# Optimization experiments

Measured on AMD Instinct MI355X. Metric: run time of the kernel, lower is better.

The kernel has to match this reference:

```python
import jax, jax.numpy as jnp
import numpy as np

B, S, H = 2, 1024, 2048
NH, NKV, HD = 16, 4, 128
KB = 1024
THETA = 10000.0
NREP = NH // NKV
NEG = -1e9


def rotate_half(x):
    x1, x2 = x[..., : HD // 2], x[..., HD // 2 :]
    return jnp.concatenate((-x2, x1), axis=-1)


def setup_inputs() -> dict:
    key = jax.random.key(0)
    ks = jax.random.split(key, 9)
    wscale = 1.0 / np.sqrt(H)
    hidden_states = jax.random.normal(ks[0], (B, S, H), dtype=jnp.float32)
    # causal additive mask over the self-attention block only
    causal = jnp.tril(jnp.ones((S, S), dtype=bool))
    attention_mask = jnp.where(causal, 0.0, NEG).astype(jnp.float32)
    attention_mask = jnp.broadcast_to(attention_mask[None, None], (B, 1, S, S))
    position_ids = jnp.broadcast_to(jnp.arange(S, dtype=jnp.int32)[None], (B, S))
    kb_keys = jax.random.normal(ks[1], (B, KB, NKV * HD), dtype=jnp.float32)
    kb_values = jax.random.normal(ks[2], (B, KB, NKV * HD), dtype=jnp.float32)
    Wq = jax.random.normal(ks[3], (NH * HD, H), dtype=jnp.float32) * wscale
    Wq_new = jax.random.normal(ks[4], (NH * HD, H), dtype=jnp.float32) * wscale
    Wk = jax.random.normal(ks[5], (NKV * HD, H), dtype=jnp.float32) * wscale
    Wv = jax.random.normal(ks[6], (NKV * HD, H), dtype=jnp.float32) * wscale
    Wo = jax.random.normal(ks[7], (H, NH * HD), dtype=jnp.float32) * wscale
    return {
        'hidden_states': hidden_states, 'attention_mask': attention_mask,
        'position_ids': position_ids, 'kb_keys': kb_keys, 'kb_values': kb_values,
        'Wq': Wq, 'Wq_new': Wq_new, 'Wk': Wk, 'Wv': Wv, 'Wo': Wo,
    }


def _rope(position_ids, dtype):
    inv_freq = 1.0 / (THETA ** (jnp.arange(0, HD, 2, dtype=jnp.float32) / HD))
    freqs = position_ids.astype(jnp.float32)[:, :, None] * inv_freq[None, None, :]  # (B,S,HD/2)
    emb = jnp.concatenate((freqs, freqs), axis=-1)  # (B,S,HD)
    return jnp.cos(emb).astype(dtype)[:, None], jnp.sin(emb).astype(dtype)[:, None]  # (B,1,S,HD)


def reference(hidden_states, attention_mask, position_ids, kb_keys, kb_values,
              Wq, Wq_new, Wk, Wv, Wo):
    x = hidden_states
    q = jnp.einsum('bsh,dh->bsd', x, Wq).reshape(B, S, NH, HD).transpose(0, 2, 1, 3)
    q_new = jnp.einsum('bsh,dh->bsd', x, Wq_new).reshape(B, S, NH, HD).transpose(0, 2, 1, 3)
    k = jnp.einsum('bsh,dh->bsd', x, Wk).reshape(B, S, NKV, HD).transpose(0, 2, 1, 3)
    v = jnp.einsum('bsh,dh->bsd', x, Wv).reshape(B, S, NKV, HD).transpose(0, 2, 1, 3)

    cos, sin = _rope(position_ids, x.dtype)
    q = q * cos + rotate_half(q) * sin          # roped self queries
    k = k * cos + rotate_half(k) * sin          # roped self keys; q_new / KB keys stay un-roped

    # GQA repeat of KV heads
    k = jnp.repeat(k, NREP, axis=1)             # (B,NH,S,HD)
    v = jnp.repeat(v, NREP, axis=1)
    kb_k = jnp.repeat(kb_keys.reshape(B, KB, NKV, HD).transpose(0, 2, 1, 3), NREP, axis=1)   # (B,NH,KB,HD)
    kb_v = jnp.repeat(kb_values.reshape(B, KB, NKV, HD).transpose(0, 2, 1, 3), NREP, axis=1)

    scale = 1.0 / np.sqrt(HD)
    scores_kb = jnp.einsum('bhqd,bhkd->bhqk', q_new, kb_k) * scale      # (B,NH,S,KB)
    scores_self = jnp.einsum('bhqd,bhkd->bhqk', q, k) * scale + attention_mask  # (B,NH,S,S)
    scores = jnp.concatenate((scores_kb, scores_self), axis=-1)          # (B,NH,S,KB+S)
    attn = jax.nn.softmax(scores, axis=-1)

    v_full = jnp.concatenate((kb_v, v), axis=2)                          # (B,NH,KB+S,HD)
    out = jnp.einsum('bhqk,bhkd->bhqd', attn, v_full)                    # (B,NH,S,HD)
    out = out.transpose(0, 2, 1, 3).reshape(B, S, NH * HD)
    return jnp.einsum('bsd,hd->bsh', out, Wo)
```

## Files before the change

### kernel.cpp

```cpp
#include <hip/hip_runtime.h>

#define Bc   2
#define Sc   1024
#define Hc   2048
#define NHc  16
#define NKVc 4
#define HDc  128
#define KBc  1024
#define NREPc 4

typedef unsigned short ushort_t;
typedef unsigned int uint32;
typedef __attribute__((ext_vector_type(8))) __bf16 bf16x8;
typedef __attribute__((ext_vector_type(4))) float f32x4;

static __device__ __forceinline__ size_t dsz(int x) { return (size_t)x; }

static __device__ __forceinline__ ushort_t f2bf(float f) {
  uint32 u = __float_as_uint(f);
  u += 0x7fffu + ((u >> 16) & 1u);
  return (ushort_t)(u >> 16);
}
static __device__ __forceinline__ float bf2f(ushort_t u) {
  return __uint_as_float(((uint32)u) << 16);
}

#define ROPE_INV 0.14391156831212787f
#define QSCALE   (0.08838834764831845f * 1.4426950408889634f)

#define FSEG 1048576
__global__ void conv_all(const float* __restrict__ x,  const float* __restrict__ Wq,
                         const float* __restrict__ Wqn, const float* __restrict__ Wk,
                         const float* __restrict__ Wv,  const float* __restrict__ Wo,
                         ushort_t* xb, ushort_t* Wqb, ushort_t* Wqnb,
                         ushort_t* Wkb, ushort_t* Wvb, ushort_t* Wob)
{
  int i = blockIdx.x * 256 + threadIdx.x;
  const float* s; ushort_t* d; int off;
  if      (i <     FSEG)            { s = x;   d = xb;   off = i; }
  else if (i < 2 * FSEG)            { s = Wq;  d = Wqb;  off = i - FSEG; }
  else if (i < 3 * FSEG)            { s = Wqn; d = Wqnb; off = i - 2 * FSEG; }
  else if (i < 3 * FSEG + FSEG / 4) { s = Wk;  d = Wkb;  off = i - 3 * FSEG; }
  else if (i < 3 * FSEG + FSEG / 2) { s = Wv;  d = Wvb;  off = i - 3 * FSEG - FSEG / 4; }
  else                              { s = Wo;  d = Wob;  off = i - 3 * FSEG - FSEG / 2; }
  float4 v = ((const float4*)s)[off];
  ushort4 o;
  o.x = f2bf(v.x); o.y = f2bf(v.y); o.z = f2bf(v.z); o.w = f2bf(v.w);
  ((ushort4*)d)[off] = o;
}

#define GL16(gsrc, ldst)                                                \
  __builtin_amdgcn_global_load_lds(                                     \
      (const __attribute__((address_space(1))) void*)(gsrc),            \
      (__attribute__((address_space(3))) void*)(ldst), 16, 0, 0)

__global__ __launch_bounds__(256) void gemm_proj(
    const ushort_t* __restrict__ A,
    const ushort_t* __restrict__ Wqb,  const ushort_t* __restrict__ Wqnb,
    const ushort_t* __restrict__ Wkb,  const ushort_t* __restrict__ Wvb,
    ushort_t* __restrict__ qb, ushort_t* __restrict__ qnb,
    ushort_t* __restrict__ kkvb, ushort_t* __restrict__ vkvb)
{
  __shared__ ushort_t sA[128 * 32];
  __shared__ ushort_t sB[128 * 32];

  const int K = Hc;
  const int bx = blockIdx.x;
  const ushort_t* Bseg; ushort_t* Cseg; int segN, colseg; float scale;
  if      (bx < 16) { Bseg = Wqb;  Cseg = qb;   segN = 2048; colseg = bx * 128;        scale = 1.f; }
  else if (bx < 32) { Bseg = Wqnb; Cseg = qnb;  segN = 2048; colseg = (bx - 16) * 128; scale = QSCALE; }
  else if (bx < 36) { Bseg = Wkb;  Cseg = kkvb; segN = 512;  colseg = (bx - 32) * 128; scale = 1.f; }
  else              { Bseg = Wvb;  Cseg = vkvb; segN = 512;  colseg = (bx - 36) * 128; scale = 1.f; }

  const int tid  = threadIdx.x;
  const int lane = tid & 63;
  const int wid  = tid >> 6;
  const int wr   = wid >> 1;
  const int wc   = wid & 1;
  const int row0 = blockIdx.y * 128;
  const int fr = lane & 15;
  const int fq = lane >> 4;

  f32x4 acc[4][4];
  #pragma unroll
  for (int m = 0; m < 4; ++m)
    #pragma unroll
    for (int n = 0; n < 4; ++n) acc[m][n] = (f32x4){0.f, 0.f, 0.f, 0.f};

  const int rS = tid >> 2;
  const int kg = (tid & 3) * 8;
  const ushort_t* Asrc0 = A + dsz(row0 + rS) * K + kg;
  const ushort_t* Asrc1 = A + dsz(row0 + 64 + rS) * K + kg;
  const ushort_t* Bsrc0 = Bseg + dsz(colseg + rS) * K + kg;
  const ushort_t* Bsrc1 = Bseg + dsz(colseg + 64 + rS) * K + kg;
  char* ldsA0 = (char*)sA + tid * 16;
  char* ldsA1 = (char*)sA + 4096 + tid * 16;
  char* ldsB0 = (char*)sB + tid * 16;
  char* ldsB1 = (char*)sB + 4096 + tid * 16;

  for (int k0 = 0; k0 < K; k0 += 32) {
    GL16(Asrc0 + k0, ldsA0);
    GL16(Asrc1 + k0, ldsA1);
    GL16(Bsrc0 + k0, ldsB0);
    GL16(Bsrc1 + k0, ldsB1);
    __syncthreads();

    bf16x8 a[4], b[4];
    #pragma unroll
    for (int m = 0; m < 4; ++m)
      a[m] = *(const bf16x8*)&sA[(wr * 64 + m * 16 + fr) * 32 + fq * 8];
    #pragma unroll
    for (int n = 0; n < 4; ++n)
      b[n] = *(const bf16x8*)&sB[(wc * 64 + n * 16 + fr) * 32 + fq * 8];
    #pragma unroll
    for (int m = 0; m < 4; ++m)
      #pragma unroll
      for (int n = 0; n < 4; ++n)
        acc[m][n] = __builtin_amdgcn_mfma_f32_16x16x32_bf16(a[m], b[n], acc[m][n], 0, 0, 0);
    __syncthreads();
  }

  #pragma unroll
  for (int m = 0; m < 4; ++m)
    #pragma unroll
    for (int n = 0; n < 4; ++n)
      #pragma unroll
      for (int j = 0; j < 4; ++j)
        Cseg[dsz(row0 + wr * 64 + m * 16 + fq * 4 + j) * segN +
             colseg + wc * 64 + n * 16 + fr] = f2bf(acc[m][n][j] * scale);
}

__global__ __launch_bounds__(256) void gemm_bt_bf16(
    const ushort_t* __restrict__ A, const ushort_t* __restrict__ B,
    float* __restrict__ C, int M, int N, int K)
{
  __shared__ ushort_t sA[128 * 32];
  __shared__ ushort_t sB[128 * 32];

  const int tid  = threadIdx.x;
  const int lane = tid & 63;
  const int wid  = tid >> 6;
  const int wr   = wid >> 1;
  const int wc   = wid & 1;
  const int row0 = blockIdx.y * 128;
  const int col0 = blockIdx.x * 128;
  const int fr = lane & 15;
  const int fq = lane >> 4;

  f32x4 acc[4][4];
  #pragma unroll
  for (int m = 0; m < 4; ++m)
    #pragma unroll
    for (int n = 0; n < 4; ++n) acc[m][n] = (f32x4){0.f, 0.f, 0.f, 0.f};

  const int rS = tid >> 2;
  const int kg = (tid & 3) * 8;
  const ushort_t* Asrc0 = A + dsz(row0 + rS) * K + kg;
  const ushort_t* Asrc1 = A + dsz(row0 + 64 + rS) * K + kg;
  const ushort_t* Bsrc0 = B + dsz(col0 + rS) * K + kg;
  const ushort_t* Bsrc1 = B + dsz(col0 + 64 + rS) * K + kg;
  char* ldsA0 = (char*)sA + tid * 16;
  char* ldsA1 = (char*)sA + 4096 + tid * 16;
  char* ldsB0 = (char*)sB + tid * 16;
  char* ldsB1 = (char*)sB + 4096 + tid * 16;

  for (int k0 = 0; k0 < K; k0 += 32) {
    GL16(Asrc0 + k0, ldsA0);
    GL16(Asrc1 + k0, ldsA1);
    GL16(Bsrc0 + k0, ldsB0);
    GL16(Bsrc1 + k0, ldsB1);
    __syncthreads();

    bf16x8 a[4], b[4];
    #pragma unroll
    for (int m = 0; m < 4; ++m)
      a[m] = *(const bf16x8*)&sA[(wr * 64 + m * 16 + fr) * 32 + fq * 8];
    #pragma unroll
    for (int n = 0; n < 4; ++n)
      b[n] = *(const bf16x8*)&sB[(wc * 64 + n * 16 + fr) * 32 + fq * 8];
    #pragma unroll
    for (int m = 0; m < 4; ++m)
      #pragma unroll
      for (int n = 0; n < 4; ++n)
        acc[m][n] = __builtin_amdgcn_mfma_f32_16x16x32_bf16(a[m], b[n], acc[m][n], 0, 0, 0);
    __syncthreads();
  }

  #pragma unroll
  for (int m = 0; m < 4; ++m)
    #pragma unroll
    for (int n = 0; n < 4; ++n)
      #pragma unroll
      for (int j = 0; j < 4; ++j)
        C[dsz(row0 + wr * 64 + m * 16 + fq * 4 + j) * N +
          col0 + wc * 64 + n * 16 + fr] = acc[m][n][j];
}

__global__ void rope_q_ip(ushort_t* __restrict__ qb, const int* __restrict__ pos)
{
  int idx = blockIdx.x * blockDim.x + threadIdx.x;
  int j = idx & 63;
  int h = (idx >> 6) & 15;
  int r = idx >> 10;
  float p = (float)pos[r];
  float f = p * expf(-(float)j * ROPE_INV);
  float c = cosf(f), s = sinf(f);
  ushort_t* d = qb + dsz(r) * (NHc * HDc) + h * HDc;
  float x1 = bf2f(d[j]), x2 = bf2f(d[j + 64]);
  d[j]      = f2bf((x1 * c - x2 * s) * QSCALE);
  d[j + 64] = f2bf((x2 * c + x1 * s) * QSCALE);
}

__global__ void rope_k_kcat(const ushort_t* __restrict__ kkvb, const int* __restrict__ pos,
                            ushort_t* __restrict__ Kcat)
{
  int idx = blockIdx.x * blockDim.x + threadIdx.x;
  int j = idx & 63;
  int kvh = (idx >> 6) & 3;
  int s = (idx >> 8) & 1023;
  int b = idx >> 18;
  float p = (float)pos[b * Sc + s];
  float f = p * expf(-(float)j * ROPE_INV);
  float c = cosf(f), sn = sinf(f);
  const ushort_t* src = kkvb + dsz(b * Sc + s) * (NKVc * HDc) + kvh * HDc;
  ushort_t* dst = Kcat + (dsz(b * NKVc + kvh) * 2048 + 1024 + s) * HDc;
  float x1 = bf2f(src[j]), x2 = bf2f(src[j + 64]);
  dst[j]      = f2bf(x1 * c - x2 * sn);
  dst[j + 64] = f2bf(x2 * c + x1 * sn);
}

__global__ void kb_kcat(const float* __restrict__ src, ushort_t* __restrict__ Kcat)
{
  int i = blockIdx.x * blockDim.x + threadIdx.x;
  int d4 = i & 31;
  int kvh = (i >> 5) & 3;
  int k = (i >> 7) & 1023;
  int b = i >> 17;
  float4 v = *(const float4*)&src[dsz(b * KBc + k) * (NKVc * HDc) + kvh * HDc + d4 * 4];
  ushort4 o;
  o.x = f2bf(v.x); o.y = f2bf(v.y); o.z = f2bf(v.z); o.w = f2bf(v.w);
  *(ushort4*)&Kcat[(dsz(b * NKVc + kvh) * 2048 + k) * HDc + d4 * 4] = o;
}

__global__ __launch_bounds__(256) void vt_build(const float* __restrict__ kbv,
                                                const ushort_t* __restrict__ vkvb,
                                                ushort_t* __restrict__ Vt)
{
  __shared__ float sT[32][33];
  const int k0 = blockIdx.x * 32;
  const int d0 = blockIdx.y * 32;
  const int bk = blockIdx.z;
  const int b = bk >> 2, kvh = bk & 3;
  const int tid = threadIdx.x;

  #pragma unroll
  for (int t = 0; t < 4; ++t) {
    int li = tid + t * 256;
    int kk = li >> 5, dl = li & 31;
    int kg = k0 + kk;
    float v = (kg < 1024)
      ? kbv[dsz(b * KBc + kg) * (NKVc * HDc) + kvh * HDc + d0 + dl]
      : bf2f(vkvb[dsz(b * Sc + kg - 1024) * (NKVc * HDc) + kvh * HDc + d0 + dl]);
    sT[kk][dl] = v;
  }
  __syncthreads();
  #pragma unroll
  for (int t = 0; t < 4; ++t) {
    int li = tid + t * 256;
    int dl = li >> 5, kk = li & 31;
    Vt[(dsz(b * NKVc + kvh) * HDc + d0 + dl) * 2048 + k0 + kk] = f2bf(sT[kk][dl]);
  }
}

__global__ __launch_bounds__(512, 2) void attn_mfma6(
    const ushort_t* __restrict__ Qr,
    const ushort_t* __restrict__ Qn,
    const ushort_t* __restrict__ Kcat,
    const ushort_t* __restrict__ Vt,
    ushort_t* __restrict__ Opart,
    float* __restrict__ mlpart)
{
  __shared__ ushort_t sK[2][32 * 128];
  __shared__ ushort_t sV[2][128 * 32];

  const int tid = threadIdx.x;
  const int lane = tid & 63;
  const int w = tid >> 6;
  const int fr = lane & 15;
  const int fq = lane >> 4;
  const int blk = blockIdx.x;
  const int third = blockIdx.y;
  const int qt = blk & 7;
  const int h  = (blk >> 3) & 15;
  const int b  = blk >> 7;
  const int kvh = h >> 2;
  const int qrow = qt * 128 + w * 16 + fr;
  const int kperm = ((fr >> 2) << 3) + (fr & 3);

  const ushort_t* Kb = Kcat + dsz(b * NKVc + kvh) * 2048 * HDc;
  const ushort_t* Vb = Vt   + dsz(b * NKVc + kvh) * HDc * 2048;

  const int nt  = 36 + 4 * qt;
  const int q3 = nt / 3, r3 = nt % 3;
  const int t_lo = third * q3 + (third < r3 ? third : r3);
  const int t_hi = t_lo + q3 + (third < r3 ? 1 : 0);

  const int krr = tid >> 4;
  const int kss = tid & 15;
  const int kuu = (krr & 3) | ((krr >> 3) << 2);
  const int kOff = krr * 256 + ((kss ^ kuu) * 16);
  const int vrr = tid >> 2;
  const int vss = tid & 3;
  const size_t vOff = (size_t)vrr * 4096 + (((vss ^ ((vrr >> 1) & 3))) * 16);

  const int vslot = (fq ^ ((fr >> 1) & 3)) * 8;

#define STAGE(bi, t)                                                   \
  {                                                                    \
    const char* kgb = (const char*)Kb + (size_t)(t) * 8192;            \
    const char* vgb = (const char*)Vb + (size_t)(t) * 64;              \
    GL16(kgb + kOff, (char*)&sK[bi][0] + tid * 16);                    \
    GL16(vgb + vOff, (char*)&sV[bi][0] + tid * 16);                    \
  }

  bf16x8 qf[4];
  {
    const ushort_t* qp = (t_lo >= 32 ? Qr : Qn) + dsz(b * Sc + qrow) * (NHc * HDc) + h * HDc;
    #pragma unroll
    for (int c = 0; c < 4; ++c) qf[c] = *(const bf16x8*)&qp[c * 32 + fq * 8];
  }

  float m = -1e30f, l = 0.f;
  f32x4 ot[8];
  #pragma unroll
  for (int dt = 0; dt < 8; ++dt) ot[dt] = (f32x4){0.f, 0.f, 0.f, 0.f};

  STAGE(0, t_lo);
  __syncthreads();

  for (int t = t_lo; t < t_hi; ++t) {
    const int cur = (t - t_lo) & 1;
    if (t + 1 < t_hi) STAGE(cur ^ 1, t + 1);

    if (t == 32) {
      const ushort_t* qp = Qr + dsz(b * Sc + qrow) * (NHc * HDc) + h * HDc;
      #pragma unroll
      for (int c = 0; c < 4; ++c) qf[c] = *(const bf16x8*)&qp[c * 32 + fq * 8];
    }
    const bool self = (t >= 32);

    bf16x8 ka0[4], ka1[4], va[8];
    #pragma unroll
    for (int c = 0; c < 4; ++c) {
      const int ks = ((c * 4 + fq) ^ fr) * 8;
      ka0[c] = *(const bf16x8*)&sK[cur][kperm * 128 + ks];
      ka1[c] = *(const bf16x8*)&sK[cur][(kperm + 4) * 128 + ks];
    }
    #pragma unroll
    for (int dt = 0; dt < 8; ++dt)
      va[dt] = *(const bf16x8*)&sV[cur][(dt * 16 + fr) * 32 + vslot];

    f32x4 s0 = (f32x4){0.f, 0.f, 0.f, 0.f};
    f32x4 s1 = (f32x4){0.f, 0.f, 0.f, 0.f};
    #pragma unroll
    for (int c = 0; c < 4; ++c)
      s0 = __builtin_amdgcn_mfma_f32_16x16x32_bf16(ka0[c], qf[c], s0, 0, 0, 0);
    #pragma unroll
    for (int c = 0; c < 4; ++c)
      s1 = __builtin_amdgcn_mfma_f32_16x16x32_bf16(ka1[c], qf[c], s1, 0, 0, 0);

    if (self) {
      #pragma unroll
      for (int j = 0; j < 4; ++j) {
        s0[j] = (t * 32 + fq * 8 + j     - 1024 > qrow) ? -1e30f : s0[j];
        s1[j] = (t * 32 + fq * 8 + 4 + j - 1024 > qrow) ? -1e30f : s1[j];
      }
    }
    float tmax = fmaxf(fmaxf(fmaxf(s0[0], s0[1]), fmaxf(s0[2], s0[3])),
                       fmaxf(fmaxf(s1[0], s1[1]), fmaxf(s1[2], s1[3])));
    tmax = fmaxf(tmax, __shfl_xor(tmax, 16));
    tmax = fmaxf(tmax, __shfl_xor(tmax, 32));

    if (__any(tmax > m + 8.f)) {
      float mnew = fmaxf(m, tmax);
      float corr = exp2f(m - mnew);
      l *= corr;
      #pragma unroll
      for (int dt = 0; dt < 8; ++dt) {
        ot[dt][0] *= corr; ot[dt][1] *= corr;
        ot[dt][2] *= corr; ot[dt][3] *= corr;
      }
      m = mnew;
    }
    float ps = 0.f;
    bf16x8 pb;
    #pragma unroll
    for (int j = 0; j < 4; ++j) { float p = exp2f(s0[j] - m); ps += p; pb[j] = (__bf16)p; }
    #pragma unroll
    for (int j = 0; j < 4; ++j) { float p = exp2f(s1[j] - m); ps += p; pb[j + 4] = (__bf16)p; }
    l += ps;

    #pragma unroll
    for (int dt = 0; dt < 8; ++dt)
      ot[dt] = __builtin_amdgcn_mfma_f32_16x16x32_bf16(va[dt], pb, ot[dt], 0, 0, 0);

    __syncthreads();
  }
#undef STAGE

  l += __shfl_xor(l, 16);
  l += __shfl_xor(l, 32);

  const int qin = w * 16 + fr;
  ushort_t* ob = Opart + (dsz(third * 256 + blk) * 128 + qin) * 128;
  #pragma unroll
  for (int dt = 0; dt < 8; ++dt) {
    ushort_t o4a[4];
    #pragma unroll
    for (int j = 0; j < 4; ++j) o4a[j] = f2bf(ot[dt][j]);
    *(ushort4*)&ob[dt * 16 + fq * 4] = *(ushort4*)o4a;
  }
  if (fq == 0) {
    float* mlp = mlpart + (dsz(third * 256 + blk) * 128 + qin) * 2;
    mlp[0] = m;
    mlp[1] = l;
  }
}

__global__ void attn_merge(const ushort_t* __restrict__ Opart,
                           const float* __restrict__ mlpart,
                           ushort_t* __restrict__ attnb)
{
  const int i = blockIdx.x * 256 + threadIdx.x;
  const int e = i * 8;
  const int qg = e >> 7;
  const int d0 = e & 127;
  const int blk = qg >> 7;
  const int qin = qg & 127;
  const int qt = blk & 7;
  const int h  = (blk >> 3) & 15;
  const int b  = blk >> 7;

  float mm[3], ll[3];
  #pragma unroll
  for (int p = 0; p < 3; ++p) {
    const float* ml = mlpart + (dsz(p * 256 + blk) * 128 + qin) * 2;
    mm[p] = ml[0]; ll[p] = ml[1];
  }
  float M = fmaxf(fmaxf(mm[0], mm[1]), mm[2]);
  float sc[3], L = 0.f;
  #pragma unroll
  for (int p = 0; p < 3; ++p) { sc[p] = exp2f(mm[p] - M); L += ll[p] * sc[p]; }
  const float Linv = 1.f / L;
  #pragma unroll
  for (int p = 0; p < 3; ++p) sc[p] *= Linv;

  float acc[8];
  #pragma unroll
  for (int j = 0; j < 8; ++j) acc[j] = 0.f;
  #pragma unroll
  for (int p = 0; p < 3; ++p) {
    const ushort_t* o = Opart + (dsz(p * 256 + blk) * 128 + qin) * 128 + d0;
    ushort4 a0 = *(const ushort4*)&o[0];
    ushort4 a1 = *(const ushort4*)&o[4];
    acc[0] += bf2f(a0.x) * sc[p]; acc[1] += bf2f(a0.y) * sc[p];
    acc[2] += bf2f(a0.z) * sc[p]; acc[3] += bf2f(a0.w) * sc[p];
    acc[4] += bf2f(a1.x) * sc[p]; acc[5] += bf2f(a1.y) * sc[p];
    acc[6] += bf2f(a1.z) * sc[p]; acc[7] += bf2f(a1.w) * sc[p];
  }

  ushort_t r[8];
  #pragma unroll
  for (int j = 0; j < 8; ++j) r[j] = f2bf(acc[j]);
  ushort_t* dst = attnb + dsz(b * Sc + qt * 128 + qin) * (NHc * HDc) + h * HDc + d0;
  *(ushort4*)&dst[0] = *(ushort4*)&r[0];
  *(ushort4*)&dst[4] = *(ushort4*)&r[4];
}

extern "C" void kernel_launch(void* const* d_in, const int* in_sizes, int n_in,
                              void* d_out, int out_size, void* d_ws, size_t ws_size,
                              hipStream_t stream)
{
  const float* x    = (const float*)d_in[0];
  const int*   pos  = (const int*)d_in[2];
  const float* kbk  = (const float*)d_in[3];
  const float* kbv  = (const float*)d_in[4];
  const float* Wq   = (const float*)d_in[5];
  const float* Wqn  = (const float*)d_in[6];
  const float* Wk   = (const float*)d_in[7];
  const float* Wv   = (const float*)d_in[8];
  const float* Wo   = (const float*)d_in[9];
  float* out = (float*)d_out;

  const int MR = Bc * Sc;
  const size_t MU = 1048576;

  ushort_t* U = (ushort_t*)d_ws;
  ushort_t* xb    = U;
  ushort_t* Wqb   = U + 4  * MU;
  ushort_t* Wqnb  = U + 8  * MU;
  ushort_t* Wkb   = U + 12 * MU;
  ushort_t* Wvb   = U + 13 * MU;
  ushort_t* Wob   = U + 14 * MU;
  ushort_t* qb    = U + 18 * MU;
  ushort_t* qnb   = U + 22 * MU;
  ushort_t* kkvb  = U + 26 * MU;
  ushort_t* vkvb  = U + 27 * MU;
  ushort_t* Kcat  = U + 28 * MU;
  ushort_t* Vt    = U + 30 * MU;
  ushort_t* attnb = U + 32 * MU;
  ushort_t* Opart  = U;
  float*    mlpart = (float*)(U + 26 * MU);

  dim3 blk(256);

  conv_all<<<18432, blk, 0, stream>>>(x, Wq, Wqn, Wk, Wv, Wo,
                                      xb, Wqb, Wqnb, Wkb, Wvb, Wob);
  gemm_proj<<<dim3(40, 16), blk, 0, stream>>>(xb, Wqb, Wqnb, Wkb, Wvb,
                                              qb, qnb, kkvb, vkvb);
  rope_q_ip<<<8192, blk, 0, stream>>>(qb, pos);
  kb_kcat<<<1024, blk, 0, stream>>>(kbk, Kcat);
  rope_k_kcat<<<2048, blk, 0, stream>>>(kkvb, pos, Kcat);
  vt_build<<<dim3(64, 4, 8), blk, 0, stream>>>(kbv, vkvb, Vt);
  attn_mfma6<<<dim3(256, 3), dim3(512), 0, stream>>>(qb, qnb, Kcat, Vt, Opart, mlpart);
  attn_merge<<<2048, blk, 0, stream>>>(Opart, mlpart, attnb);
  gemm_bt_bf16<<<dim3(16, 16), blk, 0, stream>>>(attnb, Wob, out, MR, 2048, Hc);
}
```

Measured before the change: 198.4 us.

## Split-K output GEMM, swizzle GEMM block order, precompute RoPE table

```diff
diff --git a/kernel.cpp b/kernel.cpp
--- a/kernel.cpp
+++ b/kernel.cpp
@@ -64,8 +64,12 @@
   __shared__ ushort_t sA[128 * 32];
   __shared__ ushort_t sB[128 * 32];
 
+  const int id = blockIdx.y * 40 + blockIdx.x;
+  const int sw = (id & 7) * 80 + (id >> 3);
+  const int bx = sw % 40;
+  const int by = sw / 40;
+
   const int K = Hc;
-  const int bx = blockIdx.x;
   const ushort_t* Bseg; ushort_t* Cseg; int segN, colseg; float scale;
   if      (bx < 16) { Bseg = Wqb;  Cseg = qb;   segN = 2048; colseg = bx * 128;        scale = 1.f; }
   else if (bx < 32) { Bseg = Wqnb; Cseg = qnb;  segN = 2048; colseg = (bx - 16) * 128; scale = QSCALE; }
@@ -77,7 +81,7 @@
   const int wid  = tid >> 6;
   const int wr   = wid >> 1;
   const int wc   = wid & 1;
-  const int row0 = blockIdx.y * 128;
+  const int row0 = by * 128;
   const int fr = lane & 15;
   const int fq = lane >> 4;
 
@@ -130,20 +134,29 @@
              colseg + wc * 64 + n * 16 + fr] = f2bf(acc[m][n][j] * scale);
 }
 
-__global__ __launch_bounds__(256) void gemm_bt_bf16(
+__global__ __launch_bounds__(256) void gemm_bt_splitk(
     const ushort_t* __restrict__ A, const ushort_t* __restrict__ B,
-    float* __restrict__ C, int M, int N, int K)
+    float* __restrict__ P0, float* __restrict__ P1)
 {
   __shared__ ushort_t sA[128 * 32];
   __shared__ ushort_t sB[128 * 32];
 
+  const int id = (blockIdx.z * 16 + blockIdx.y) * 16 + blockIdx.x;
+  const int sw = (id & 7) * 64 + (id >> 3);
+  const int bx = sw & 15;
+  const int by = (sw >> 4) & 15;
+  const int bz = sw >> 8;
+
+  const int K = Hc;
   const int tid  = threadIdx.x;
   const int lane = tid & 63;
   const int wid  = tid >> 6;
   const int wr   = wid >> 1;
   const int wc   = wid & 1;
-  const int row0 = blockIdx.y * 128;
-  const int col0 = blockIdx.x * 128;
+  const int row0 = by * 128;
+  const int col0 = bx * 128;
+  const int koff = bz * 1024;
+  float* C = bz ? P1 : P0;
   const int fr = lane & 15;
   const int fq = lane >> 4;
 
@@ -155,16 +168,16 @@
 
   const int rS = tid >> 2;
   const int kg = (tid & 3) * 8;
-  const ushort_t* Asrc0 = A + dsz(row0 + rS) * K + kg;
-  const ushort_t* Asrc1 = A + dsz(row0 + 64 + rS) * K + kg;
-  const ushort_t* Bsrc0 = B + dsz(col0 + rS) * K + kg;
-  const ushort_t* Bsrc1 = B + dsz(col0 + 64 + rS) * K + kg;
+  const ushort_t* Asrc0 = A + dsz(row0 + rS) * K + koff + kg;
+  const ushort_t* Asrc1 = A + dsz(row0 + 64 + rS) * K + koff + kg;
+  const ushort_t* Bsrc0 = B + dsz(col0 + rS) * K + koff + kg;
+  const ushort_t* Bsrc1 = B + dsz(col0 + 64 + rS) * K + koff + kg;
   char* ldsA0 = (char*)sA + tid * 16;
   char* ldsA1 = (char*)sA + 4096 + tid * 16;
   char* ldsB0 = (char*)sB + tid * 16;
   char* ldsB1 = (char*)sB + 4096 + tid * 16;
 
-  for (int k0 = 0; k0 < K; k0 += 32) {
+  for (int k0 = 0; k0 < 1024; k0 += 32) {
     GL16(Asrc0 + k0, ldsA0);
     GL16(Asrc1 + k0, ldsA1);
     GL16(Bsrc0 + k0, ldsB0);
@@ -192,26 +205,45 @@
     for (int n = 0; n < 4; ++n)
       #pragma unroll
       for (int j = 0; j < 4; ++j)
-        C[dsz(row0 + wr * 64 + m * 16 + fq * 4 + j) * N +
+        C[dsz(row0 + wr * 64 + m * 16 + fq * 4 + j) * 2048 +
           col0 + wc * 64 + n * 16 + fr] = acc[m][n][j];
 }
 
-__global__ void rope_q_ip(ushort_t* __restrict__ qb, const int* __restrict__ pos)
+__global__ void add_partials(const float* __restrict__ P0, const float* __restrict__ P1,
+                             float* __restrict__ out)
+{
+  int i = blockIdx.x * 256 + threadIdx.x;
+  float4 a = ((const float4*)P0)[i];
+  float4 b = ((const float4*)P1)[i];
+  float4 r; r.x = a.x + b.x; r.y = a.y + b.y; r.z = a.z + b.z; r.w = a.w + b.w;
+  ((float4*)out)[i] = r;
+}
+
+__global__ void rope_tab(const int* __restrict__ pos, float2* __restrict__ tab)
+{
+  int idx = blockIdx.x * 256 + threadIdx.x;
+  int j = idx & 63;
+  int r = idx >> 6;
+  float p = (float)pos[r];
+  float f = p * expf(-(float)j * ROPE_INV);
+  float2 cs; cs.x = cosf(f); cs.y = sinf(f);
+  tab[idx] = cs;
+}
+
+__global__ void rope_q_ip(ushort_t* __restrict__ qb, const float2* __restrict__ tab)
 {
   int idx = blockIdx.x * blockDim.x + threadIdx.x;
   int j = idx & 63;
   int h = (idx >> 6) & 15;
   int r = idx >> 10;
-  float p = (float)pos[r];
-  float f = p * expf(-(float)j * ROPE_INV);
-  float c = cosf(f), s = sinf(f);
+  float2 cs = tab[r * 64 + j];
   ushort_t* d = qb + dsz(r) * (NHc * HDc) + h * HDc;
   float x1 = bf2f(d[j]), x2 = bf2f(d[j + 64]);
-  d[j]      = f2bf((x1 * c - x2 * s) * QSCALE);
-  d[j + 64] = f2bf((x2 * c + x1 * s) * QSCALE);
-}
-
-__global__ void rope_k_kcat(const ushort_t* __restrict__ kkvb, const int* __restrict__ pos,
+  d[j]      = f2bf((x1 * cs.x - x2 * cs.y) * QSCALE);
+  d[j + 64] = f2bf((x2 * cs.x + x1 * cs.y) * QSCALE);
+}
+
+__global__ void rope_k_kcat(const ushort_t* __restrict__ kkvb, const float2* __restrict__ tab,
                             ushort_t* __restrict__ Kcat)
 {
   int idx = blockIdx.x * blockDim.x + threadIdx.x;
@@ -219,14 +251,12 @@
   int kvh = (idx >> 6) & 3;
   int s = (idx >> 8) & 1023;
   int b = idx >> 18;
-  float p = (float)pos[b * Sc + s];
-  float f = p * expf(-(float)j * ROPE_INV);
-  float c = cosf(f), sn = sinf(f);
+  float2 cs = tab[(b * Sc + s) * 64 + j];
   const ushort_t* src = kkvb + dsz(b * Sc + s) * (NKVc * HDc) + kvh * HDc;
   ushort_t* dst = Kcat + (dsz(b * NKVc + kvh) * 2048 + 1024 + s) * HDc;
   float x1 = bf2f(src[j]), x2 = bf2f(src[j + 64]);
-  dst[j]      = f2bf(x1 * c - x2 * sn);
-  dst[j + 64] = f2bf(x2 * c + x1 * sn);
+  dst[j]      = f2bf(x1 * cs.x - x2 * cs.y);
+  dst[j + 64] = f2bf(x2 * cs.x + x1 * cs.y);
 }
 
 __global__ void kb_kcat(const float* __restrict__ src, ushort_t* __restrict__ Kcat)
@@ -492,7 +522,6 @@
   const float* Wo   = (const float*)d_in[9];
   float* out = (float*)d_out;
 
-  const int MR = Bc * Sc;
   const size_t MU = 1048576;
 
   ushort_t* U = (ushort_t*)d_ws;
@@ -511,6 +540,9 @@
   ushort_t* attnb = U + 32 * MU;
   ushort_t* Opart  = U;
   float*    mlpart = (float*)(U + 26 * MU);
+  float2*   ropet  = (float2*)(U + 12 * MU);
+  float*    P0     = (float*)U;
+  float*    P1     = (float*)(U + 18 * MU);
 
   dim3 blk(256);
 
@@ -518,11 +550,13 @@
                                       xb, Wqb, Wqnb, Wkb, Wvb, Wob);
   gemm_proj<<<dim3(40, 16), blk, 0, stream>>>(xb, Wqb, Wqnb, Wkb, Wvb,
                                               qb, qnb, kkvb, vkvb);
-  rope_q_ip<<<8192, blk, 0, stream>>>(qb, pos);
+  rope_tab<<<512, blk, 0, stream>>>(pos, ropet);
+  rope_q_ip<<<8192, blk, 0, stream>>>(qb, ropet);
   kb_kcat<<<1024, blk, 0, stream>>>(kbk, Kcat);
-  rope_k_kcat<<<2048, blk, 0, stream>>>(kkvb, pos, Kcat);
+  rope_k_kcat<<<2048, blk, 0, stream>>>(kkvb, ropet, Kcat);
   vt_build<<<dim3(64, 4, 8), blk, 0, stream>>>(kbv, vkvb, Vt);
   attn_mfma6<<<dim3(256, 3), dim3(512), 0, stream>>>(qb, qnb, Kcat, Vt, Opart, mlpart);
   attn_merge<<<2048, blk, 0, stream>>>(Opart, mlpart, attnb);
-  gemm_bt_bf16<<<dim3(16, 16), blk, 0, stream>>>(attnb, Wob, out, MR, 2048, Hc);
-}
+  gemm_bt_splitk<<<dim3(16, 16, 2), blk, 0, stream>>>(attnb, Wob, P0, P1);
+  add_partials<<<4096, blk, 0, stream>>>(P0, P1, out);
+}
```

Result: faster. 189.6 us (median of 2 runs) (-4.4%).
